# Performance work log

Hardware: AMD Instinct MI355X
Metric: run time of the kernel (lower is better)

## Reference

```python
import jax, jax.numpy as jnp
from jax import lax
import numpy as np

B, C, Hf, Wf = 4, 256, 64, 64
COMP = max(C // 4, 16)  # 64
SCALE, K_UP, K_ENC = 2, 5, 3
EPS = 1e-5


def setup_inputs() -> dict:
    key = jax.random.key(0)
    ks = jax.random.split(key, 6)
    x = jax.random.normal(ks[0], (B, C, Hf, Wf), dtype=jnp.float32)
    w_comp = jax.random.normal(ks[1], (COMP, C), dtype=jnp.float32) * (1.0 / np.sqrt(C))
    bn_gamma = jnp.ones((COMP,), dtype=jnp.float32)
    bn_beta = jnp.zeros((COMP,), dtype=jnp.float32)
    bn_mean = jax.random.normal(ks[2], (COMP,), dtype=jnp.float32) * 0.1
    bn_var = jax.random.uniform(ks[3], (COMP,), dtype=jnp.float32, minval=0.5, maxval=1.5)
    w_enc = jax.random.normal(ks[4], (K_UP * K_UP * SCALE * SCALE, COMP, K_ENC, K_ENC), dtype=jnp.float32) * (1.0 / np.sqrt(COMP * K_ENC * K_ENC))
    return {"x": x, "w_comp": w_comp, "bn_gamma": bn_gamma, "bn_beta": bn_beta,
            "bn_mean": bn_mean, "bn_var": bn_var, "w_enc": w_enc}


def reference(x, w_comp, bn_gamma, bn_beta, bn_mean, bn_var, w_enc):
    b, c, h, w = x.shape
    s, k = SCALE, K_UP
    # 1x1 compression conv
    comp = jnp.einsum('bchw,oc->bohw', x, w_comp)
    # BatchNorm (eval-style, running stats) + SiLU
    inv = (bn_gamma / jnp.sqrt(bn_var + EPS))[:, None, None]
    bn = (comp - bn_mean[:, None, None]) * inv + bn_beta[:, None, None]
    act = bn * jax.nn.sigmoid(bn)
    # encoder conv -> per-pixel reassembly kernels, channels = k^2 * s^2 (k2 outer, s2 inner)
    mask = lax.conv_general_dilated(act, w_enc, (1, 1), ((1, 1), (1, 1)),
                                    dimension_numbers=('NCHW', 'OIHW', 'NCHW'))
    mask = mask.reshape(b, k * k, s * s, h, w)
    mask = jax.nn.softmax(mask, axis=1)  # softmax over k_up*k_up window
    # unfold: gather 5x5 neighborhoods (pad 2), k = dy*5+dx row-major like F.unfold
    pad = k // 2
    xp = jnp.pad(x, ((0, 0), (0, 0), (pad, pad), (pad, pad)))
    patches = jnp.stack([xp[:, :, dy:dy + h, dx:dx + w]
                         for dy in range(k) for dx in range(k)], axis=2)  # (b,c,k2,h,w)
    # content-aware weighted sum per sub-pixel position
    out = jnp.einsum('bksij,bckij->bcsij', mask, patches)  # (b,c,s2,h,w)
    # s2 -> (s0,s1); pixel (i*s+s0, j*s+s1)
    out = out.reshape(b, c, s, s, h, w).transpose(0, 1, 4, 2, 5, 3).reshape(b, c, h * s, w * s)
    return out
```

## Files before the change

### kernel.cpp

```cpp
#include <hip/hip_runtime.h>
#include <hip/hip_bf16.h>
#include <hip/hip_fp16.h>
#include <math.h>

#define B_ 4
#define C_ 256
#define H_ 64
#define W_ 64
#define COMP_ 64
#define K2_ 25
#define HW_ (H_*W_)
#define EPS_ 1e-5f
#define WTE_STRIDE 26

typedef float v2f __attribute__((ext_vector_type(2)));
#define FMA2(a, b, c) __builtin_elementwise_fma((a), (b), (c))

__global__ void k_transpose(const float* __restrict__ w_comp,
                            const float* __restrict__ w_enc,
                            float* __restrict__ wTc,
                            float* __restrict__ wTe) {
    int t = blockIdx.x * 256 + threadIdx.x;
    if (t < COMP_ * C_) {
        int o = t & 63;
        int c = t >> 6;
        wTc[t] = w_comp[o * C_ + c];
    } else {
        int t2 = t - COMP_ * C_;
        if (t2 < 100 * COMP_ * 9) {
            int k2 = t2 % 25;
            int r = t2 / 25;
            int s2 = r & 3; r >>= 2;
            int q = r % 9;
            int o = r / 9;
            wTe[((o * 9 + q) * 4 + s2) * WTE_STRIDE + k2] =
                w_enc[(((k2 * 4 + s2) * COMP_) + o) * 9 + q];
        }
    }
}

__global__ void __launch_bounds__(1024)
k_compress(const float* __restrict__ x, const float* __restrict__ wTc,
           const float* __restrict__ gamma, const float* __restrict__ beta,
           const float* __restrict__ mean, const float* __restrict__ var,
           float* __restrict__ act) {
    __shared__ v2f red[32 * 64];
    const int tx = threadIdx.x;
    const int ty = threadIdx.y;
    const int tz = threadIdx.z;
    const int ogu = __builtin_amdgcn_readfirstlane(ty);
    const int cgu = __builtin_amdgcn_readfirstlane(tz);
    const int b = blockIdx.y;
    const int p0 = blockIdx.x * 64;

    v2f acc2[4];
#pragma unroll
    for (int k = 0; k < 4; ++k) acc2[k] = (v2f){0.f, 0.f};

    const float* xb = x + (size_t)b * C_ * HW_ + p0 + tx;
#pragma unroll 8
    for (int cl = 0; cl < 128; ++cl) {
        int c = cgu * 128 + cl;
        float xv = xb[c * HW_];
        const v2f* w2 = (const v2f*)(wTc + c * COMP_ + ogu * 8);
        v2f xv2 = (v2f){xv, xv};
#pragma unroll
        for (int k = 0; k < 4; ++k)
            acc2[k] = FMA2(xv2, w2[k], acc2[k]);
    }

    if (tz == 1) {
#pragma unroll
        for (int k = 0; k < 4; ++k) red[(ty * 4 + k) * 64 + tx] = acc2[k];
    }
    __syncthreads();
    if (tz == 0) {
#pragma unroll
        for (int k = 0; k < 4; ++k) {
            v2f s = acc2[k] + red[(ty * 4 + k) * 64 + tx];
            int o0 = ty * 8 + 2 * k;
#pragma unroll
            for (int h = 0; h < 2; ++h) {
                int o = o0 + h;
                float sv = (h == 0) ? s.x : s.y;
                float iv = gamma[o] * rsqrtf(var[o] + EPS_);
                float bn = (sv - mean[o]) * iv + beta[o];
                float sg = 1.f / (1.f + __expf(-bn));
                act[((b * COMP_ + o) * HW_) + p0 + tx] = bn * sg;
            }
        }
    }
}

__global__ void __launch_bounds__(1024)
k_encoder(const float* __restrict__ act, const float* __restrict__ wTe,
          __half* __restrict__ maskT) {
    __shared__ float sact[13312];
    const int tx = threadIdx.x;
    const int ty = threadIdx.y;
    const int tz = threadIdx.z;
    const int tid = (tz * 4 + ty) * 64 + tx;
    const int i = blockIdx.x;
    const int b = blockIdx.y;
    const int s2u = __builtin_amdgcn_readfirstlane(ty);
    const int ogu = __builtin_amdgcn_readfirstlane(tz);

    const float* ab = act + (size_t)b * COMP_ * HW_;
    for (int t = tid; t < 3 * COMP_ * 66; t += 1024) {
        int col = t % 66;
        int r = t / 66;
        int o = r & 63;
        int row = r >> 6;
        int gi = i + row - 1;
        int gj = col - 1;
        float v = 0.f;
        if ((unsigned)gi < 64u && (unsigned)gj < 64u)
            v = ab[(o * H_ + gi) * W_ + gj];
        sact[t] = v;
    }
    __syncthreads();

    v2f acc2[13];
#pragma unroll
    for (int k = 0; k < 13; ++k) acc2[k] = (v2f){0.f, 0.f};

#pragma unroll 2
    for (int oi = 0; oi < 16; ++oi) {
        int o = ogu * 16 + oi;
#pragma unroll
        for (int q = 0; q < 9; ++q) {
            const int dy = q / 3, dx = q % 3;
            float a = sact[(dy * COMP_ + o) * 66 + tx + dx];
            const float* wb = wTe + ((o * 9 + q) * 4 + s2u) * WTE_STRIDE;
            const v2f* w2 = (const v2f*)wb;
            v2f a2 = (v2f){a, a};
#pragma unroll
            for (int k = 0; k < 12; ++k)
                acc2[k] = FMA2(a2, w2[k], acc2[k]);
            acc2[12].x = fmaf(wb[24], a, acc2[12].x);
        }
    }
    __syncthreads();

    v2f* bufA = (v2f*)sact;
    v2f* bufB = bufA + 3328;
    const int rix = ty * 64 + tx;
    if (tz == 1) {
#pragma unroll
        for (int k = 0; k < 13; ++k) bufA[k * 256 + rix] = acc2[k];
    } else if (tz == 2) {
#pragma unroll
        for (int k = 0; k < 13; ++k) bufB[k * 256 + rix] = acc2[k];
    }
    __syncthreads();
    if (tz == 0) {
#pragma unroll
        for (int k = 0; k < 13; ++k) acc2[k] += bufA[k * 256 + rix];
    } else if (tz == 3) {
#pragma unroll
        for (int k = 0; k < 13; ++k) acc2[k] += bufB[k * 256 + rix];
    }
    __syncthreads();
    if (tz == 3) {
#pragma unroll
        for (int k = 0; k < 13; ++k) bufA[k * 256 + rix] = acc2[k];
    }
    __syncthreads();
    float ex[K2_];
    if (tz == 0) {
#pragma unroll
        for (int k = 0; k < 13; ++k) acc2[k] += bufA[k * 256 + rix];

        float mx = acc2[12].x;
#pragma unroll
        for (int k = 0; k < 12; ++k) mx = fmaxf(mx, fmaxf(acc2[k].x, acc2[k].y));
        float sum = 0.f;
#pragma unroll
        for (int k = 0; k < 12; ++k) {
            ex[2 * k]     = __expf(acc2[k].x - mx);
            ex[2 * k + 1] = __expf(acc2[k].y - mx);
            sum += ex[2 * k] + ex[2 * k + 1];
        }
        ex[24] = __expf(acc2[12].x - mx);
        sum += ex[24];
        float rs = 1.f / sum;
#pragma unroll
        for (int k = 0; k < K2_; ++k) ex[k] *= rs;
    }
    __syncthreads();

    __half* st = (__half*)sact;
    if (tz == 0) {
#pragma unroll
        for (int k = 0; k < K2_; ++k)
            st[tx * 100 + k * 4 + ty] = __float2half(ex[k]);
    }
    __syncthreads();

    float4* dst = (float4*)(maskT + ((size_t)b * HW_ + i * 64) * 100);
    const float4* src = (const float4*)st;
    if (tid < 800) dst[tid] = src[tid];
}

__global__ void __launch_bounds__(256)
k_reassemble(const float* __restrict__ x, const __half* __restrict__ maskT,
             float* __restrict__ out) {
    __shared__ __align__(16) __half smask[64 * 100];
    __shared__ __align__(16) float sx[5 * 68 * 20];
    const int tx = threadIdx.x;
    const int ty = threadIdx.y;
    const int tid = ty * 64 + tx;
    const int i = blockIdx.x;
    const int cc = blockIdx.y;
    const int b = blockIdx.z;

    {
        const float4* src = (const float4*)(maskT + ((size_t)b * HW_ + i * 64) * 100);
        float4* dst = (float4*)smask;
#pragma unroll
        for (int t = 0; t < 4; ++t) {
            int e = tid + t * 256;
            if (e < 800) dst[e] = src[e];
        }
    }

    const float* xb = x + ((size_t)b * C_ + cc * 16 + ty * 4) * HW_;
#pragma unroll
    for (int r = 0; r < 5; ++r) {
        const int gi = i + r - 2;
        const bool rowok = ((unsigned)gi < 64u);
        {
            float4 v = {0.f, 0.f, 0.f, 0.f};
            int gj = tx - 2;
            if (rowok && gj >= 0) {
                const float* p = xb + gi * W_ + gj;
                v.x = p[0];
                v.y = p[HW_];
                v.z = p[2 * HW_];
                v.w = p[3 * HW_];
            }
            *(float4*)&sx[(r * 68 + tx) * 20 + ty * 4] = v;
        }
        if (tid < 16) {
            int q = tid >> 2;
            int col = 64 + (tid & 3);
            int gj = col - 2;
            float4 v = {0.f, 0.f, 0.f, 0.f};
            if (rowok && gj < 64) {
                const float* p = x + ((size_t)b * C_ + cc * 16 + q * 4) * HW_ + gi * W_ + gj;
                v.x = p[0];
                v.y = p[HW_];
                v.z = p[2 * HW_];
                v.w = p[3 * HW_];
            }
            *(float4*)&sx[(r * 68 + col) * 20 + q * 4] = v;
        }
    }
    __syncthreads();

    v2f a01[4], a23[4];
#pragma unroll
    for (int cl = 0; cl < 4; ++cl) { a01[cl] = (v2f){0.f, 0.f}; a23[cl] = (v2f){0.f, 0.f}; }

    float4 xq = *(const float4*)&sx[(0 * 68 + tx + 0) * 20 + ty * 4];
    __half2 h01 = *(const __half2*)&smask[tx * 100 + 0];
    __half2 h23 = *(const __half2*)&smask[tx * 100 + 2];

#pragma unroll
    for (int k2 = 0; k2 < K2_; ++k2) {
        float4 xq_c = xq;
        __half2 h01_c = h01, h23_c = h23;
        if (k2 < K2_ - 1) {
            const int kn = k2 + 1;
            const int dy = kn / 5, dx = kn % 5;
            xq  = *(const float4*)&sx[(dy * 68 + tx + dx) * 20 + ty * 4];
            h01 = *(const __half2*)&smask[tx * 100 + kn * 4];
            h23 = *(const __half2*)&smask[tx * 100 + kn * 4 + 2];
        }
        float2 f01 = __half22float2(h01_c);
        float2 f23 = __half22float2(h23_c);
        v2f m01 = (v2f){f01.x, f01.y};
        v2f m23 = (v2f){f23.x, f23.y};
        float xc[4] = {xq_c.x, xq_c.y, xq_c.z, xq_c.w};
#pragma unroll
        for (int cl = 0; cl < 4; ++cl) {
            v2f xv2 = (v2f){xc[cl], xc[cl]};
            a01[cl] = FMA2(xv2, m01, a01[cl]);
            a23[cl] = FMA2(xv2, m23, a23[cl]);
        }
    }

#pragma unroll
    for (int cl = 0; cl < 4; ++cl) {
        int c = cc * 16 + ty * 4 + cl;
        float* op = out + (((size_t)(b * C_ + c) * 128 + 2 * i) * 128) + 2 * tx;
        *(float2*)op         = float2{a01[cl].x, a01[cl].y};
        *(float2*)(op + 128) = float2{a23[cl].x, a23[cl].y};
    }
}

extern "C" void kernel_launch(void* const* d_in, const int* in_sizes, int n_in,
                              void* d_out, int out_size, void* d_ws, size_t ws_size,
                              hipStream_t stream) {
    const float* x       = (const float*)d_in[0];
    const float* w_comp  = (const float*)d_in[1];
    const float* bn_g    = (const float*)d_in[2];
    const float* bn_b    = (const float*)d_in[3];
    const float* bn_m    = (const float*)d_in[4];
    const float* bn_v    = (const float*)d_in[5];
    const float* w_enc   = (const float*)d_in[6];
    float* out = (float*)d_out;

    float* ws    = (float*)d_ws;
    float* wTc   = ws;
    float* wTe   = ws + 16384;
    float* act   = ws + 16384 + 59904;
    __half* maskT = (__half*)(act + (size_t)B_ * COMP_ * HW_);

    k_transpose<<<289, 256, 0, stream>>>(w_comp, w_enc, wTc, wTe);
    k_compress<<<dim3(64, B_), dim3(64, 8, 2), 0, stream>>>(x, wTc, bn_g, bn_b, bn_m, bn_v, act);
    k_encoder<<<dim3(64, B_), dim3(64, 4, 4), 0, stream>>>(act, wTe, maskT);
    k_reassemble<<<dim3(64, 16, B_), dim3(64, 4), 0, stream>>>(x, maskT, out);
}
```

Measured before the change: 168.9 us.

## Split compress/encoder blocks across output groups and widen reassemble channel tiles

```diff
diff --git a/kernel.cpp b/kernel.cpp
--- a/kernel.cpp
+++ b/kernel.cpp
@@ -39,18 +39,19 @@
     }
 }
 
-__global__ void __launch_bounds__(1024)
+__global__ void __launch_bounds__(512)
 k_compress(const float* __restrict__ x, const float* __restrict__ wTc,
            const float* __restrict__ gamma, const float* __restrict__ beta,
            const float* __restrict__ mean, const float* __restrict__ var,
            float* __restrict__ act) {
-    __shared__ v2f red[32 * 64];
+    __shared__ v2f red[16 * 64];
     const int tx = threadIdx.x;
     const int ty = threadIdx.y;
     const int tz = threadIdx.z;
     const int ogu = __builtin_amdgcn_readfirstlane(ty);
     const int cgu = __builtin_amdgcn_readfirstlane(tz);
-    const int b = blockIdx.y;
+    const int ogH = blockIdx.y;
+    const int b = blockIdx.z;
     const int p0 = blockIdx.x * 64;
 
     v2f acc2[4];
@@ -62,7 +63,7 @@
     for (int cl = 0; cl < 128; ++cl) {
         int c = cgu * 128 + cl;
         float xv = xb[c * HW_];
-        const v2f* w2 = (const v2f*)(wTc + c * COMP_ + ogu * 8);
+        const v2f* w2 = (const v2f*)(wTc + c * COMP_ + ogH * 32 + ogu * 8);
         v2f xv2 = (v2f){xv, xv};
 #pragma unroll
         for (int k = 0; k < 4; ++k)
@@ -78,7 +79,7 @@
 #pragma unroll
         for (int k = 0; k < 4; ++k) {
             v2f s = acc2[k] + red[(ty * 4 + k) * 64 + tx];
-            int o0 = ty * 8 + 2 * k;
+            int o0 = ogH * 32 + ty * 8 + 2 * k;
 #pragma unroll
             for (int h = 0; h < 2; ++h) {
                 int o = o0 + h;
@@ -92,21 +93,22 @@
     }
 }
 
-__global__ void __launch_bounds__(1024)
+__global__ void __launch_bounds__(512)
 k_encoder(const float* __restrict__ act, const float* __restrict__ wTe,
           __half* __restrict__ maskT) {
-    __shared__ float sact[13312];
+    __shared__ float sact[12672];
     const int tx = threadIdx.x;
     const int ty = threadIdx.y;
     const int tz = threadIdx.z;
-    const int tid = (tz * 4 + ty) * 64 + tx;
+    const int tid = (tz * 2 + ty) * 64 + tx;
     const int i = blockIdx.x;
-    const int b = blockIdx.y;
-    const int s2u = __builtin_amdgcn_readfirstlane(ty);
+    const int sg = blockIdx.y;
+    const int b = blockIdx.z;
+    const int s2u = sg * 2 + __builtin_amdgcn_readfirstlane(ty);
     const int ogu = __builtin_amdgcn_readfirstlane(tz);
 
     const float* ab = act + (size_t)b * COMP_ * HW_;
-    for (int t = tid; t < 3 * COMP_ * 66; t += 1024) {
+    for (int t = tid; t < 3 * COMP_ * 66; t += 512) {
         int col = t % 66;
         int r = t / 66;
         int o = r & 63;
@@ -142,34 +144,20 @@
     }
     __syncthreads();
 
-    v2f* bufA = (v2f*)sact;
-    v2f* bufB = bufA + 3328;
+    v2f* bufs = (v2f*)sact;
     const int rix = ty * 64 + tx;
-    if (tz == 1) {
-#pragma unroll
-        for (int k = 0; k < 13; ++k) bufA[k * 256 + rix] = acc2[k];
-    } else if (tz == 2) {
-#pragma unroll
-        for (int k = 0; k < 13; ++k) bufB[k * 256 + rix] = acc2[k];
-    }
-    __syncthreads();
-    if (tz == 0) {
-#pragma unroll
-        for (int k = 0; k < 13; ++k) acc2[k] += bufA[k * 256 + rix];
-    } else if (tz == 3) {
-#pragma unroll
-        for (int k = 0; k < 13; ++k) acc2[k] += bufB[k * 256 + rix];
-    }
-    __syncthreads();
-    if (tz == 3) {
-#pragma unroll
-        for (int k = 0; k < 13; ++k) bufA[k * 256 + rix] = acc2[k];
+    if (tz != 0) {
+#pragma unroll
+        for (int k = 0; k < 13; ++k)
+            bufs[(tz - 1) * 1664 + k * 128 + rix] = acc2[k];
     }
     __syncthreads();
     float ex[K2_];
     if (tz == 0) {
 #pragma unroll
-        for (int k = 0; k < 13; ++k) acc2[k] += bufA[k * 256 + rix];
+        for (int k = 0; k < 13; ++k)
+            acc2[k] += bufs[k * 128 + rix] + bufs[1664 + k * 128 + rix] +
+                       bufs[2 * 1664 + k * 128 + rix];
 
         float mx = acc2[12].x;
 #pragma unroll
@@ -193,20 +181,23 @@
     if (tz == 0) {
 #pragma unroll
         for (int k = 0; k < K2_; ++k)
-            st[tx * 100 + k * 4 + ty] = __float2half(ex[k]);
-    }
-    __syncthreads();
-
-    float4* dst = (float4*)(maskT + ((size_t)b * HW_ + i * 64) * 100);
-    const float4* src = (const float4*)st;
-    if (tid < 800) dst[tid] = src[tid];
+            st[tx * 100 + k * 4 + sg * 2 + ty] = __float2half(ex[k]);
+    }
+    __syncthreads();
+
+    const unsigned* st32 = (const unsigned*)st;
+    unsigned* dst = (unsigned*)(maskT + ((size_t)b * HW_ + i * 64) * 100);
+    for (int e = tid; e < 1600; e += 512) {
+        int j = e / 25, k = e - j * 25;
+        dst[j * 50 + k * 2 + sg] = st32[j * 50 + k * 2 + sg];
+    }
 }
 
 __global__ void __launch_bounds__(256)
 k_reassemble(const float* __restrict__ x, const __half* __restrict__ maskT,
              float* __restrict__ out) {
     __shared__ __align__(16) __half smask[64 * 100];
-    __shared__ __align__(16) float sx[5 * 68 * 20];
+    __shared__ __align__(16) float sx[5 * 68 * 36];
     const int tx = threadIdx.x;
     const int ty = threadIdx.y;
     const int tid = ty * 64 + tx;
@@ -224,75 +215,75 @@
         }
     }
 
-    const float* xb = x + ((size_t)b * C_ + cc * 16 + ty * 4) * HW_;
+    const float* xc0 = x + ((size_t)b * C_ + cc * 32) * HW_;
 #pragma unroll
     for (int r = 0; r < 5; ++r) {
         const int gi = i + r - 2;
         const bool rowok = ((unsigned)gi < 64u);
         {
-            float4 v = {0.f, 0.f, 0.f, 0.f};
             int gj = tx - 2;
+            float4 va = {0.f, 0.f, 0.f, 0.f};
+            float4 vb = {0.f, 0.f, 0.f, 0.f};
             if (rowok && gj >= 0) {
-                const float* p = xb + gi * W_ + gj;
-                v.x = p[0];
-                v.y = p[HW_];
-                v.z = p[2 * HW_];
-                v.w = p[3 * HW_];
+                const float* p = xc0 + (ty * 8) * HW_ + gi * W_ + gj;
+                va.x = p[0];        va.y = p[HW_];
+                va.z = p[2 * HW_];  va.w = p[3 * HW_];
+                vb.x = p[4 * HW_];  vb.y = p[5 * HW_];
+                vb.z = p[6 * HW_];  vb.w = p[7 * HW_];
             }
-            *(float4*)&sx[(r * 68 + tx) * 20 + ty * 4] = v;
-        }
-        if (tid < 16) {
-            int q = tid >> 2;
+            *(float4*)&sx[(r * 68 + tx) * 36 + ty * 8]     = va;
+            *(float4*)&sx[(r * 68 + tx) * 36 + ty * 8 + 4] = vb;
+        }
+        if (tid < 32) {
+            int quad = tid >> 2;
             int col = 64 + (tid & 3);
             int gj = col - 2;
             float4 v = {0.f, 0.f, 0.f, 0.f};
             if (rowok && gj < 64) {
-                const float* p = x + ((size_t)b * C_ + cc * 16 + q * 4) * HW_ + gi * W_ + gj;
-                v.x = p[0];
-                v.y = p[HW_];
-                v.z = p[2 * HW_];
-                v.w = p[3 * HW_];
+                const float* p = xc0 + (quad * 4) * HW_ + gi * W_ + gj;
+                v.x = p[0];       v.y = p[HW_];
+                v.z = p[2 * HW_]; v.w = p[3 * HW_];
             }
-            *(float4*)&sx[(r * 68 + col) * 20 + q * 4] = v;
-        }
-    }
-    __syncthreads();
-
-    v2f a01[4], a23[4];
-#pragma unroll
-    for (int cl = 0; cl < 4; ++cl) { a01[cl] = (v2f){0.f, 0.f}; a23[cl] = (v2f){0.f, 0.f}; }
-
-    float4 xq = *(const float4*)&sx[(0 * 68 + tx + 0) * 20 + ty * 4];
-    __half2 h01 = *(const __half2*)&smask[tx * 100 + 0];
-    __half2 h23 = *(const __half2*)&smask[tx * 100 + 2];
+            *(float4*)&sx[(r * 68 + col) * 36 + quad * 4] = v;
+        }
+    }
+    __syncthreads();
+
+    v2f a01[8], a23[8];
+#pragma unroll
+    for (int cl = 0; cl < 8; ++cl) { a01[cl] = (v2f){0.f, 0.f}; a23[cl] = (v2f){0.f, 0.f}; }
+
+    float4 xqA = *(const float4*)&sx[(0 * 68 + tx) * 36 + ty * 8];
+    float4 xqB = *(const float4*)&sx[(0 * 68 + tx) * 36 + ty * 8 + 4];
+    uint2 mu = *(const uint2*)&smask[tx * 100];
 
 #pragma unroll
     for (int k2 = 0; k2 < K2_; ++k2) {
-        float4 xq_c = xq;
-        __half2 h01_c = h01, h23_c = h23;
+        float4 xA = xqA, xB = xqB;
+        uint2 mc = mu;
         if (k2 < K2_ - 1) {
             const int kn = k2 + 1;
             const int dy = kn / 5, dx = kn % 5;
-            xq  = *(const float4*)&sx[(dy * 68 + tx + dx) * 20 + ty * 4];
-            h01 = *(const __half2*)&smask[tx * 100 + kn * 4];
-            h23 = *(const __half2*)&smask[tx * 100 + kn * 4 + 2];
-        }
-        float2 f01 = __half22float2(h01_c);
-        float2 f23 = __half22float2(h23_c);
+            xqA = *(const float4*)&sx[(dy * 68 + tx + dx) * 36 + ty * 8];
+            xqB = *(const float4*)&sx[(dy * 68 + tx + dx) * 36 + ty * 8 + 4];
+            mu  = *(const uint2*)&smask[tx * 100 + kn * 4];
+        }
+        float2 f01 = __half22float2(__builtin_bit_cast(__half2, mc.x));
+        float2 f23 = __half22float2(__builtin_bit_cast(__half2, mc.y));
         v2f m01 = (v2f){f01.x, f01.y};
         v2f m23 = (v2f){f23.x, f23.y};
-        float xc[4] = {xq_c.x, xq_c.y, xq_c.z, xq_c.w};
-#pragma unroll
-        for (int cl = 0; cl < 4; ++cl) {
-            v2f xv2 = (v2f){xc[cl], xc[cl]};
+        float xcv[8] = {xA.x, xA.y, xA.z, xA.w, xB.x, xB.y, xB.z, xB.w};
+#pragma unroll
+        for (int cl = 0; cl < 8; ++cl) {
+            v2f xv2 = (v2f){xcv[cl], xcv[cl]};
             a01[cl] = FMA2(xv2, m01, a01[cl]);
             a23[cl] = FMA2(xv2, m23, a23[cl]);
         }
     }
 
 #pragma unroll
-    for (int cl = 0; cl < 4; ++cl) {
-        int c = cc * 16 + ty * 4 + cl;
+    for (int cl = 0; cl < 8; ++cl) {
+        int c = cc * 32 + ty * 8 + cl;
         float* op = out + (((size_t)(b * C_ + c) * 128 + 2 * i) * 128) + 2 * tx;
         *(float2*)op         = float2{a01[cl].x, a01[cl].y};
         *(float2*)(op + 128) = float2{a23[cl].x, a23[cl].y};
@@ -318,7 +309,7 @@
     __half* maskT = (__half*)(act + (size_t)B_ * COMP_ * HW_);
 
     k_transpose<<<289, 256, 0, stream>>>(w_comp, w_enc, wTc, wTe);
-    k_compress<<<dim3(64, B_), dim3(64, 8, 2), 0, stream>>>(x, wTc, bn_g, bn_b, bn_m, bn_v, act);
-    k_encoder<<<dim3(64, B_), dim3(64, 4, 4), 0, stream>>>(act, wTe, maskT);
-    k_reassemble<<<dim3(64, 16, B_), dim3(64, 4), 0, stream>>>(x, maskT, out);
-}
+    k_compress<<<dim3(64, 2, B_), dim3(64, 4, 2), 0, stream>>>(x, wTc, bn_g, bn_b, bn_m, bn_v, act);
+    k_encoder<<<dim3(64, 2, B_), dim3(64, 2, 4), 0, stream>>>(act, wTe, maskT);
+    k_reassemble<<<dim3(64, 8, B_), dim3(64, 4), 0, stream>>>(x, maskT, out);
+}
```

Measured after the change: 186.3 us. 10.3% more time.
